# Optimization experiments

Hardware: AMD Instinct MI355X
Metric: run time of the kernel (lower is better)

## Reference

```python
import jax, jax.numpy as jnp
import numpy as np

B, N, D, H = 2, 2048, 1024, 16
HD = D // H
EPS = 1e-5

def _ln(x, g, b):
    m = jnp.mean(x, axis=-1, keepdims=True)
    v = jnp.mean((x - m) ** 2, axis=-1, keepdims=True)
    return (x - m) * jax.lax.rsqrt(v + EPS) * g + b

def setup_inputs() -> dict:
    key = jax.random.key(0)
    ks = jax.random.split(key, 16)
    s = 0.02
    inp = {
        'x': jax.random.normal(ks[0], (B, N, D), jnp.float32),
        'ln1_g': jnp.ones((D,), jnp.float32), 'ln1_b': jnp.zeros((D,), jnp.float32),
        'w_in': jax.random.normal(ks[1], (D, D), jnp.float32) * s, 'b_in': jnp.zeros((D,), jnp.float32),
        'wq': jax.random.normal(ks[2], (D, D), jnp.float32) * s,
        'wk': jax.random.normal(ks[3], (D, D), jnp.float32) * s,
        'wv': jax.random.normal(ks[4], (D, D), jnp.float32) * s,
        'wo': jax.random.normal(ks[5], (D, D), jnp.float32) * s, 'bo': jnp.zeros((D,), jnp.float32),
        'ln2_g': jnp.ones((D,), jnp.float32), 'ln2_b': jnp.zeros((D,), jnp.float32),
        'w_up': jax.random.normal(ks[6], (D, 4 * D), jnp.float32) * s, 'b_up': jnp.zeros((4 * D,), jnp.float32),
        'w_gate': jax.random.normal(ks[7], (D, 4 * D), jnp.float32) * s, 'b_gate': jnp.zeros((4 * D,), jnp.float32),
        'w_down': jax.random.normal(ks[8], (4 * D, D), jnp.float32) * s, 'b_down': jnp.zeros((D,), jnp.float32),
        'top_k': 64,
    }
    return inp

def _sparse_attention(h, wq, wk, wv, wo, bo, top_k):
    q = (h @ wq).reshape(B, N, H, HD).transpose(0, 2, 1, 3)  # [B,H,N,hd]
    k = (h @ wk).reshape(B, N, H, HD).transpose(0, 2, 1, 3)
    v = (h @ wv).reshape(B, N, H, HD).transpose(0, 2, 1, 3)
    scale = HD ** -0.5
    scores = jnp.einsum('bhqd,bhkd->bhqk', q, k) * scale  # [B,H,N,N]
    if top_k < N:
        # keep top_k per row: threshold at the k-th largest score
        kth = jax.lax.top_k(scores, top_k)[0][..., -1:]
        scores = jnp.where(scores >= kth, scores, -jnp.inf)
    attn = jax.nn.softmax(scores, axis=-1)
    out = jnp.einsum('bhqk,bhkd->bhqd', attn, v)
    out = out.transpose(0, 2, 1, 3).reshape(B, N, D)
    return out @ wo + bo

def reference(x, ln1_g, ln1_b, w_in, b_in, wq, wk, wv, wo, bo,
              ln2_g, ln2_b, w_up, b_up, w_gate, b_gate, w_down, b_down, top_k):
    h = _ln(x, ln1_g, ln1_b) @ w_in + b_in
    h = h + _sparse_attention(h, wq, wk, wv, wo, bo, top_k)
    ff_in = _ln(h, ln2_g, ln2_b)
    gate = jax.nn.silu(ff_in @ w_gate + b_gate)
    ff = (ff_in @ w_up + b_up) * gate
    ff = ff @ w_down + b_down
    return h + ff
```

## Files before the change

### kernel.cpp

```cpp
#include <hip/hip_runtime.h>
#include <cstdint>


#define DEV __device__ __forceinline__

constexpr int B_  = 2;
constexpr int N_  = 2048;
constexpr int D_  = 1024;
constexpr int H_  = 16;
constexpr int HD_ = 64;
constexpr int M_  = B_ * N_;
constexpr float EPS_ = 1e-5f;

using short8 = __attribute__((ext_vector_type(8))) short;
using f32x4  = __attribute__((ext_vector_type(4))) float;

DEV float4 ld4(const float* p) { return *reinterpret_cast<const float4*>(p); }
DEV void   st4(float* p, float4 v) { *reinterpret_cast<float4*>(p) = v; }

DEV unsigned short bf16r(float x) {
  unsigned u = __float_as_uint(x);
  u += 0x7fffu + ((u >> 16) & 1u);
  return (unsigned short)(u >> 16);
}
DEV float bf2f(unsigned short h) { return __uint_as_float(((unsigned)h) << 16); }

DEV unsigned fkey(float f) {
  unsigned u = __float_as_uint(f);
  return u ^ ((unsigned)((int)u >> 31) | 0x80000000u);
}
DEV float fval(unsigned k) {
  unsigned u = (k & 0x80000000u) ? (k ^ 0x80000000u) : ~k;
  return __uint_as_float(u);
}

__global__ __launch_bounds__(256) void wconv_kernel(const float* __restrict__ W,
                                                    unsigned short* __restrict__ Thi,
                                                    unsigned short* __restrict__ Tlo,
                                                    int K, int N) {
  __shared__ float t[32][33];
  const int k0 = blockIdx.y * 32, n0 = blockIdx.x * 32;
  const int tid = threadIdx.x;
  const int r = tid >> 3, c4 = (tid & 7) * 4;
  float4 v = ld4(W + (size_t)(k0 + r) * N + n0 + c4);
  t[r][c4 + 0] = v.x; t[r][c4 + 1] = v.y; t[r][c4 + 2] = v.z; t[r][c4 + 3] = v.w;
  __syncthreads();
  const int n = tid >> 3, kc = (tid & 7) * 4;
  ushort4 hv, lv;
  {
    float x0 = t[kc + 0][n], x1 = t[kc + 1][n], x2 = t[kc + 2][n], x3 = t[kc + 3][n];
    hv.x = bf16r(x0); lv.x = bf16r(x0 - bf2f(hv.x));
    hv.y = bf16r(x1); lv.y = bf16r(x1 - bf2f(hv.y));
    hv.z = bf16r(x2); lv.z = bf16r(x2 - bf2f(hv.z));
    hv.w = bf16r(x3); lv.w = bf16r(x3 - bf2f(hv.w));
  }
  *reinterpret_cast<ushort4*>(&Thi[(size_t)(n0 + n) * K + k0 + kc]) = hv;
  *reinterpret_cast<ushort4*>(&Tlo[(size_t)(n0 + n) * K + k0 + kc]) = lv;
}

__global__ __launch_bounds__(256) void ln_kernel(const float* __restrict__ in,
                                                 const float* __restrict__ g,
                                                 const float* __restrict__ b,
                                                 unsigned short* __restrict__ ohi,
                                                 unsigned short* __restrict__ olo) {
  const int row = blockIdx.x;
  const int t = threadIdx.x;
  float4 v = ld4(in + (size_t)row * D_ + t * 4);
  float s  = v.x + v.y + v.z + v.w;
  float ss = v.x * v.x + v.y * v.y + v.z * v.z + v.w * v.w;
  #pragma unroll
  for (int o = 32; o; o >>= 1) { s += __shfl_down(s, o); ss += __shfl_down(ss, o); }
  __shared__ float rs[4], rss[4];
  const int wid = t >> 6, lane = t & 63;
  if (lane == 0) { rs[wid] = s; rss[wid] = ss; }
  __syncthreads();
  s  = rs[0] + rs[1] + rs[2] + rs[3];
  ss = rss[0] + rss[1] + rss[2] + rss[3];
  const float mean = s * (1.f / D_);
  const float var  = ss * (1.f / D_) - mean * mean;
  const float rstd = rsqrtf(var + EPS_);
  float4 gv = ld4(g + t * 4);
  float4 bv = ld4(b + t * 4);
  float o0 = (v.x - mean) * rstd * gv.x + bv.x;
  float o1 = (v.y - mean) * rstd * gv.y + bv.y;
  float o2 = (v.z - mean) * rstd * gv.z + bv.z;
  float o3 = (v.w - mean) * rstd * gv.w + bv.w;
  ushort4 hv, lv;
  hv.x = bf16r(o0); lv.x = bf16r(o0 - bf2f(hv.x));
  hv.y = bf16r(o1); lv.y = bf16r(o1 - bf2f(hv.y));
  hv.z = bf16r(o2); lv.z = bf16r(o2 - bf2f(hv.z));
  hv.w = bf16r(o3); lv.w = bf16r(o3 - bf2f(hv.w));
  *reinterpret_cast<ushort4*>(&ohi[(size_t)row * D_ + t * 4]) = hv;
  *reinterpret_cast<ushort4*>(&olo[(size_t)row * D_ + t * 4]) = lv;
}

enum { GO_PAIR_BIAS = 0, GO_F32 = 1, GO_F32_BIAS_RESPAIR = 2,
       GO_F32_BIAS_RESF32 = 3, GO_F32_RES_NB = 4 };

template <int EPI>
__global__ __launch_bounds__(256) void gemm_sb(const unsigned short* __restrict__ Ah,
                                               const unsigned short* __restrict__ Al,
                                               const unsigned short* __restrict__ Bh,
                                               const unsigned short* __restrict__ Bl,
                                               const float* __restrict__ bias,
                                               const unsigned short* __restrict__ Rh,
                                               const unsigned short* __restrict__ Rl,
                                               const float* __restrict__ Rf,
                                               unsigned short* __restrict__ Ohi,
                                               unsigned short* __restrict__ Olo,
                                               float* __restrict__ Of,
                                               int M, int N, int K) {
  __shared__ unsigned short Ahs[128 * 40], Als[128 * 40];
  __shared__ unsigned short Bhs[64 * 40],  Bls[64 * 40];
  const int tid = threadIdx.x;
  const int m0 = blockIdx.y * 128, n0 = blockIdx.x * 64;
  const int lane = tid & 63, w = tid >> 6;
  const int wr = w >> 1, wc = w & 1;

  const int rA0 = tid >> 2, rA1 = 64 + (tid >> 2), chA = (tid & 3) * 8;
  const int rB = tid >> 2,  chB = (tid & 3) * 8;
  const size_t gA0 = (size_t)(m0 + rA0) * K + chA;
  const size_t gA1 = (size_t)(m0 + rA1) * K + chA;
  const size_t gB  = (size_t)(n0 + rB) * K + chB;
  const int lA0 = rA0 * 40 + chA, lA1 = rA1 * 40 + chA, lB = rB * 40 + chB;

  f32x4 acc[4][2];
  #pragma unroll
  for (int i = 0; i < 4; ++i)
    #pragma unroll
    for (int j = 0; j < 2; ++j) acc[i][j] = f32x4{0.f, 0.f, 0.f, 0.f};

  const int fr = lane & 15, fk = (lane >> 4) * 8;
  const int arow0 = (wr * 64 + fr) * 40 + fk;
  const int brow0 = (wc * 32 + fr) * 40 + fk;

  for (int k0 = 0; k0 < K; k0 += 32) {
    short8 a0h = *reinterpret_cast<const short8*>(&Ah[gA0 + k0]);
    short8 a1h = *reinterpret_cast<const short8*>(&Ah[gA1 + k0]);
    short8 a0l = *reinterpret_cast<const short8*>(&Al[gA0 + k0]);
    short8 a1l = *reinterpret_cast<const short8*>(&Al[gA1 + k0]);
    short8 bh  = *reinterpret_cast<const short8*>(&Bh[gB + k0]);
    short8 bl  = *reinterpret_cast<const short8*>(&Bl[gB + k0]);
    __syncthreads();
    *reinterpret_cast<short8*>(&Ahs[lA0]) = a0h;
    *reinterpret_cast<short8*>(&Ahs[lA1]) = a1h;
    *reinterpret_cast<short8*>(&Als[lA0]) = a0l;
    *reinterpret_cast<short8*>(&Als[lA1]) = a1l;
    *reinterpret_cast<short8*>(&Bhs[lB])  = bh;
    *reinterpret_cast<short8*>(&Bls[lB])  = bl;
    __syncthreads();

    short8 amh[4], aml[4], bnh[2], bnl[2];
    #pragma unroll
    for (int mf = 0; mf < 4; ++mf) {
      amh[mf] = *reinterpret_cast<const short8*>(&Ahs[arow0 + mf * 16 * 40]);
      aml[mf] = *reinterpret_cast<const short8*>(&Als[arow0 + mf * 16 * 40]);
    }
    #pragma unroll
    for (int nf = 0; nf < 2; ++nf) {
      bnh[nf] = *reinterpret_cast<const short8*>(&Bhs[brow0 + nf * 16 * 40]);
      bnl[nf] = *reinterpret_cast<const short8*>(&Bls[brow0 + nf * 16 * 40]);
    }
    #pragma unroll
    for (int mf = 0; mf < 4; ++mf)
      #pragma unroll
      for (int nf = 0; nf < 2; ++nf) {
        acc[mf][nf] = __builtin_amdgcn_mfma_f32_16x16x32_bf16(amh[mf], bnh[nf], acc[mf][nf], 0, 0, 0);
        acc[mf][nf] = __builtin_amdgcn_mfma_f32_16x16x32_bf16(amh[mf], bnl[nf], acc[mf][nf], 0, 0, 0);
        acc[mf][nf] = __builtin_amdgcn_mfma_f32_16x16x32_bf16(aml[mf], bnh[nf], acc[mf][nf], 0, 0, 0);
      }
  }

  const int er = (lane >> 4) * 4, ec = lane & 15;
  #pragma unroll
  for (int mf = 0; mf < 4; ++mf)
    #pragma unroll
    for (int nf = 0; nf < 2; ++nf)
      #pragma unroll
      for (int j = 0; j < 4; ++j) {
        const int m = m0 + wr * 64 + mf * 16 + er + j;
        const int n = n0 + wc * 32 + nf * 16 + ec;
        float v = acc[mf][nf][j];
        if constexpr (EPI == GO_PAIR_BIAS || EPI == GO_F32_BIAS_RESPAIR ||
                      EPI == GO_F32_BIAS_RESF32) v += bias[n];
        const size_t idx = (size_t)m * N + n;
        if constexpr (EPI == GO_PAIR_BIAS) {
          unsigned short h = bf16r(v);
          Ohi[idx] = h; Olo[idx] = bf16r(v - bf2f(h));
        } else if constexpr (EPI == GO_F32) {
          Of[idx] = v;
        } else if constexpr (EPI == GO_F32_BIAS_RESPAIR) {
          Of[idx] = v + bf2f(Rh[idx]) + bf2f(Rl[idx]);
        } else {
          Of[idx] = v + Rf[idx];
        }
      }
}

__global__ __launch_bounds__(256) void gemm_gateup(const unsigned short* __restrict__ Ah,
                                                   const unsigned short* __restrict__ Al,
                                                   const unsigned short* __restrict__ Gh,
                                                   const unsigned short* __restrict__ Gl,
                                                   const unsigned short* __restrict__ Uh,
                                                   const unsigned short* __restrict__ Ul,
                                                   const float* __restrict__ bg,
                                                   const float* __restrict__ bu,
                                                   unsigned short* __restrict__ Ohi,
                                                   unsigned short* __restrict__ Olo,
                                                   int M, int N, int K) {
  __shared__ unsigned short Ahs[128 * 40], Als[128 * 40];
  __shared__ unsigned short Ghs[64 * 40], Gls[64 * 40], Uhs[64 * 40], Uls[64 * 40];
  const int tid = threadIdx.x;
  const int m0 = blockIdx.y * 128, n0 = blockIdx.x * 64;
  const int lane = tid & 63, w = tid >> 6;
  const int wr = w >> 1, wc = w & 1;

  const int rA0 = tid >> 2, rA1 = 64 + (tid >> 2), chA = (tid & 3) * 8;
  const int rB = tid >> 2, chB = (tid & 3) * 8;
  const size_t gA0 = (size_t)(m0 + rA0) * K + chA;
  const size_t gA1 = (size_t)(m0 + rA1) * K + chA;
  const size_t gB  = (size_t)(n0 + rB) * K + chB;
  const int lA0 = rA0 * 40 + chA, lA1 = rA1 * 40 + chA, lB = rB * 40 + chB;

  f32x4 accg[4][2], accu[4][2];
  #pragma unroll
  for (int i = 0; i < 4; ++i)
    #pragma unroll
    for (int j = 0; j < 2; ++j) {
      accg[i][j] = f32x4{0.f, 0.f, 0.f, 0.f};
      accu[i][j] = f32x4{0.f, 0.f, 0.f, 0.f};
    }

  const int fr = lane & 15, fk = (lane >> 4) * 8;
  const int arow0 = (wr * 64 + fr) * 40 + fk;
  const int brow0 = (wc * 32 + fr) * 40 + fk;

  for (int k0 = 0; k0 < K; k0 += 32) {
    short8 a0h = *reinterpret_cast<const short8*>(&Ah[gA0 + k0]);
    short8 a1h = *reinterpret_cast<const short8*>(&Ah[gA1 + k0]);
    short8 a0l = *reinterpret_cast<const short8*>(&Al[gA0 + k0]);
    short8 a1l = *reinterpret_cast<const short8*>(&Al[gA1 + k0]);
    short8 gh = *reinterpret_cast<const short8*>(&Gh[gB + k0]);
    short8 gl = *reinterpret_cast<const short8*>(&Gl[gB + k0]);
    short8 uh = *reinterpret_cast<const short8*>(&Uh[gB + k0]);
    short8 ul = *reinterpret_cast<const short8*>(&Ul[gB + k0]);
    __syncthreads();
    *reinterpret_cast<short8*>(&Ahs[lA0]) = a0h;
    *reinterpret_cast<short8*>(&Ahs[lA1]) = a1h;
    *reinterpret_cast<short8*>(&Als[lA0]) = a0l;
    *reinterpret_cast<short8*>(&Als[lA1]) = a1l;
    *reinterpret_cast<short8*>(&Ghs[lB]) = gh;
    *reinterpret_cast<short8*>(&Gls[lB]) = gl;
    *reinterpret_cast<short8*>(&Uhs[lB]) = uh;
    *reinterpret_cast<short8*>(&Uls[lB]) = ul;
    __syncthreads();

    short8 amh[4], aml[4];
    #pragma unroll
    for (int mf = 0; mf < 4; ++mf) {
      amh[mf] = *reinterpret_cast<const short8*>(&Ahs[arow0 + mf * 16 * 40]);
      aml[mf] = *reinterpret_cast<const short8*>(&Als[arow0 + mf * 16 * 40]);
    }
    #pragma unroll
    for (int nf = 0; nf < 2; ++nf) {
      short8 gnh = *reinterpret_cast<const short8*>(&Ghs[brow0 + nf * 16 * 40]);
      short8 gnl = *reinterpret_cast<const short8*>(&Gls[brow0 + nf * 16 * 40]);
      short8 unh = *reinterpret_cast<const short8*>(&Uhs[brow0 + nf * 16 * 40]);
      short8 unl = *reinterpret_cast<const short8*>(&Uls[brow0 + nf * 16 * 40]);
      #pragma unroll
      for (int mf = 0; mf < 4; ++mf) {
        accg[mf][nf] = __builtin_amdgcn_mfma_f32_16x16x32_bf16(amh[mf], gnh, accg[mf][nf], 0, 0, 0);
        accg[mf][nf] = __builtin_amdgcn_mfma_f32_16x16x32_bf16(amh[mf], gnl, accg[mf][nf], 0, 0, 0);
        accg[mf][nf] = __builtin_amdgcn_mfma_f32_16x16x32_bf16(aml[mf], gnh, accg[mf][nf], 0, 0, 0);
        accu[mf][nf] = __builtin_amdgcn_mfma_f32_16x16x32_bf16(amh[mf], unh, accu[mf][nf], 0, 0, 0);
        accu[mf][nf] = __builtin_amdgcn_mfma_f32_16x16x32_bf16(amh[mf], unl, accu[mf][nf], 0, 0, 0);
        accu[mf][nf] = __builtin_amdgcn_mfma_f32_16x16x32_bf16(aml[mf], unh, accu[mf][nf], 0, 0, 0);
      }
    }
  }

  const int er = (lane >> 4) * 4, ec = lane & 15;
  #pragma unroll
  for (int mf = 0; mf < 4; ++mf)
    #pragma unroll
    for (int nf = 0; nf < 2; ++nf)
      #pragma unroll
      for (int j = 0; j < 4; ++j) {
        const int m = m0 + wr * 64 + mf * 16 + er + j;
        const int n = n0 + wc * 32 + nf * 16 + ec;
        float g = accg[mf][nf][j] + bg[n];
        float u = accu[mf][nf][j] + bu[n];
        float f = (g / (1.f + expf(-g))) * u;
        const size_t idx = (size_t)m * N + n;
        unsigned short h = bf16r(f);
        Ohi[idx] = h; Olo[idx] = bf16r(f - bf2f(h));
      }
}

__global__ __launch_bounds__(256) void attn_kernel(const float* __restrict__ qm,
                                                   const float* __restrict__ km,
                                                   const float* __restrict__ vm,
                                                   unsigned short* __restrict__ aoh,
                                                   unsigned short* __restrict__ aol,
                                                   const int* __restrict__ topk_p) {
  constexpr int QT = 4, CT = 128, NCH = N_ / CT;
  constexpr int NJ = 2 * NCH;
  __shared__ float Kc[CT][HD_];
  __shared__ float Pt[4][QT][CT];
  int*   selIdx = (int*)&Pt[0][0][0];
  float* selW   = (float*)&Pt[2][0][0];

  const int tid = threadIdx.x;
  const int bid = ((blockIdx.x & 7) << 11) | (blockIdx.x >> 3);
  const int qt = bid & (N_ / QT - 1);
  const int hh = (bid >> 9) & (H_ - 1);
  const int bb = bid >> 13;
  const int q0 = qt * QT;
  const size_t baseKV = (size_t)bb * N_ * D_ + (size_t)hh * HD_;
  const int lane = tid & 63;
  const int w = tid >> 6;
  const float scale = 0.125f;

  float4 qr[QT][4];
  #pragma unroll
  for (int r = 0; r < QT; ++r)
    #pragma unroll
    for (int dq = 0; dq < 4; ++dq) {
      float4 t = ld4(qm + baseKV + (size_t)(q0 + r) * D_ + w * 16 + dq * 4);
      t.x *= scale; t.y *= scale; t.z *= scale; t.w *= scale;
      qr[r][dq] = t;
    }

  unsigned key[NJ];
  for (int cb = 0; cb < NCH; ++cb) {
    float4 kst[8];
    #pragma unroll
    for (int it = 0; it < 8; ++it) {
      const int c = it * 16 + (tid >> 4);
      kst[it] = ld4(km + baseKV + (size_t)(cb * CT + c) * D_ + (tid & 15) * 4);
    }
    __syncthreads();
    #pragma unroll
    for (int it = 0; it < 8; ++it) {
      const int c = it * 16 + (tid >> 4);
      const int chk = (tid & 15) ^ (c & 15);
      st4(&Kc[c][chk * 4], kst[it]);
    }
    __syncthreads();

    float pa[QT][2];
    #pragma unroll
    for (int r = 0; r < QT; ++r) { pa[r][0] = 0.f; pa[r][1] = 0.f; }
    #pragma unroll
    for (int dq = 0; dq < 4; ++dq) {
      const int ch = w * 4 + dq;
      float4 k0 = ld4(&Kc[lane][(ch ^ (lane & 15)) * 4]);
      float4 k1 = ld4(&Kc[lane + 64][(ch ^ (lane & 15)) * 4]);
      #pragma unroll
      for (int r = 0; r < QT; ++r) {
        float4 qv = qr[r][dq];
        pa[r][0] += qv.x * k0.x + qv.y * k0.y + qv.z * k0.z + qv.w * k0.w;
        pa[r][1] += qv.x * k1.x + qv.y * k1.y + qv.z * k1.z + qv.w * k1.w;
      }
    }
    #pragma unroll
    for (int r = 0; r < QT; ++r) {
      Pt[w][r][lane]      = pa[r][0];
      Pt[w][r][lane + 64] = pa[r][1];
    }
    __syncthreads();
    {
      float s0 = Pt[0][w][lane] + Pt[1][w][lane] + Pt[2][w][lane] + Pt[3][w][lane];
      float s1 = Pt[0][w][lane + 64] + Pt[1][w][lane + 64] +
                 Pt[2][w][lane + 64] + Pt[3][w][lane + 64];
      key[2 * cb]     = fkey(s0);
      key[2 * cb + 1] = fkey(s1);
    }
  }

  int topk = *topk_p;
  if (topk > N_) topk = N_;

  unsigned kmax = 0;
  #pragma unroll
  for (int j = 0; j < NJ; ++j) kmax = (key[j] > kmax) ? key[j] : kmax;
  #pragma unroll
  for (int o = 32; o; o >>= 1) {
    unsigned t = __shfl_xor(kmax, o);
    kmax = (t > kmax) ? t : kmax;
  }
  const float smax = fval(kmax);

  unsigned thr = 0u;
  if (topk < N_) {
    for (int bit = 31; bit >= 0; --bit) {
      const unsigned cand = thr | (1u << bit);
      int c = 0;
      #pragma unroll
      for (int j = 0; j < NJ; ++j)
        c += __popcll(__ballot(key[j] >= cand));
      if (c >= topk) thr = cand;
    }
  }

  __syncthreads();
  int base = 0;
  float wpart = 0.f;
  #pragma unroll
  for (int j = 0; j < NJ; ++j) {
    const bool sel = key[j] >= thr;
    const unsigned long long m = __ballot(sel);
    if (sel) {
      const int pos = base + (int)__popcll(m & ((1ull << lane) - 1ull));
      if (pos < 128) {
        const float wgt = expf(fval(key[j]) - smax);
        selIdx[w * 128 + pos] = j * 64 + lane;
        selW[w * 128 + pos] = wgt;
        wpart += wgt;
      }
    }
    base += (int)__popcll(m);
  }
  int cnt = (base > 128) ? 128 : base;
  float wsum = wpart;
  #pragma unroll
  for (int o = 32; o; o >>= 1) wsum += __shfl_xor(wsum, o);

  const float* Vb = vm + baseKV;
  float outv = 0.f;
  int i = 0;
  for (; i + 16 <= cnt; i += 16) {
    int ix[16]; float wv[16], vv[16];
    #pragma unroll
    for (int t = 0; t < 16; ++t) {
      ix[t] = selIdx[w * 128 + i + t];
      wv[t] = selW[w * 128 + i + t];
    }
    #pragma unroll
    for (int t = 0; t < 16; ++t) vv[t] = Vb[(size_t)ix[t] * D_ + lane];
    #pragma unroll
    for (int t = 0; t < 16; ++t) outv += wv[t] * vv[t];
  }
  for (; i < cnt; ++i)
    outv += selW[w * 128 + i] * Vb[(size_t)selIdx[w * 128 + i] * D_ + lane];

  const float o = outv / wsum;
  const size_t oidx = ((size_t)bb * N_ + q0 + w) * D_ + hh * HD_ + lane;
  unsigned short h = bf16r(o);
  aoh[oidx] = h; aol[oidx] = bf16r(o - bf2f(h));
}

extern "C" void kernel_launch(void* const* d_in, const int* in_sizes, int n_in,
                              void* d_out, int out_size, void* d_ws, size_t ws_size,
                              hipStream_t stream) {
  const float* x      = (const float*)d_in[0];
  const float* ln1_g  = (const float*)d_in[1];
  const float* ln1_b  = (const float*)d_in[2];
  const float* w_in   = (const float*)d_in[3];
  const float* b_in   = (const float*)d_in[4];
  const float* wq     = (const float*)d_in[5];
  const float* wk     = (const float*)d_in[6];
  const float* wv     = (const float*)d_in[7];
  const float* wo     = (const float*)d_in[8];
  const float* bo     = (const float*)d_in[9];
  const float* ln2_g  = (const float*)d_in[10];
  const float* ln2_b  = (const float*)d_in[11];
  const float* w_up   = (const float*)d_in[12];
  const float* b_up   = (const float*)d_in[13];
  const float* w_gate = (const float*)d_in[14];
  const float* b_gate = (const float*)d_in[15];
  const float* w_down = (const float*)d_in[16];
  const float* b_down = (const float*)d_in[17];
  const int*   topk   = (const int*)d_in[18];
  float* out = (float*)d_out;

  char* p = (char*)d_ws;
  const size_t MB = 1024 * 1024;
  unsigned short* Wi_h = (unsigned short*)(p + 0 * MB);
  unsigned short* Wi_l = (unsigned short*)(p + 2 * MB);
  unsigned short* Wq_h = (unsigned short*)(p + 4 * MB);
  unsigned short* Wq_l = (unsigned short*)(p + 6 * MB);
  unsigned short* Wk_h = (unsigned short*)(p + 8 * MB);
  unsigned short* Wk_l = (unsigned short*)(p + 10 * MB);
  unsigned short* Wv_h = (unsigned short*)(p + 12 * MB);
  unsigned short* Wv_l = (unsigned short*)(p + 14 * MB);
  unsigned short* Wo_h = (unsigned short*)(p + 16 * MB);
  unsigned short* Wo_l = (unsigned short*)(p + 18 * MB);
  unsigned short* Wd0_h = (unsigned short*)(p + 20 * MB);
  unsigned short* Wd0_l = (unsigned short*)(p + 24 * MB);
  unsigned short* Wd1_h = (unsigned short*)(p + 28 * MB);
  unsigned short* Wd1_l = (unsigned short*)(p + 32 * MB);
  unsigned short* hp_h = (unsigned short*)(p + 36 * MB);
  unsigned short* hp_l = (unsigned short*)(p + 44 * MB);
  unsigned short* ff_h = (unsigned short*)(p + 36 * MB);
  unsigned short* ff_l = (unsigned short*)(p + 44 * MB);
  unsigned short* xn_h = (unsigned short*)(p + 52 * MB);
  unsigned short* xn_l = (unsigned short*)(p + 60 * MB);
  float*          qb   = (float*)(p + 52 * MB);
  float*          kb   = (float*)(p + 68 * MB);
  float*          vb   = (float*)(p + 84 * MB);
  unsigned short* Wg_h = (unsigned short*)(p + 52 * MB);
  unsigned short* Wg_l = (unsigned short*)(p + 60 * MB);
  unsigned short* Wu_h = (unsigned short*)(p + 68 * MB);
  unsigned short* Wu_l = (unsigned short*)(p + 76 * MB);
  unsigned short* f1_h = (unsigned short*)(p + 84 * MB);
  unsigned short* ao_h = (unsigned short*)(p + 0 * MB);
  unsigned short* ao_l = (unsigned short*)(p + 8 * MB);
  unsigned short* f1_l = (unsigned short*)(p + 0 * MB);

  const dim3 blk(256);
  const dim3 gW1k(32, 32);
  const dim3 gWgu(128, 32);
  const dim3 gWd(32, 64);
  const dim3 g1024(16, 32);
  const dim3 g2048(32, 32);

  wconv_kernel<<<gW1k, blk, 0, stream>>>(w_in, Wi_h, Wi_l, 1024, 1024);
  wconv_kernel<<<gW1k, blk, 0, stream>>>(wq, Wq_h, Wq_l, 1024, 1024);
  wconv_kernel<<<gW1k, blk, 0, stream>>>(wk, Wk_h, Wk_l, 1024, 1024);
  wconv_kernel<<<gW1k, blk, 0, stream>>>(wv, Wv_h, Wv_l, 1024, 1024);
  wconv_kernel<<<gW1k, blk, 0, stream>>>(wo, Wo_h, Wo_l, 1024, 1024);
  wconv_kernel<<<gWd, blk, 0, stream>>>(w_down,               Wd0_h, Wd0_l, 2048, 1024);
  wconv_kernel<<<gWd, blk, 0, stream>>>(w_down + 2048 * 1024, Wd1_h, Wd1_l, 2048, 1024);

  ln_kernel<<<M_, blk, 0, stream>>>(x, ln1_g, ln1_b, xn_h, xn_l);
  gemm_sb<GO_PAIR_BIAS><<<g1024, blk, 0, stream>>>(xn_h, xn_l, Wi_h, Wi_l, b_in,
      nullptr, nullptr, nullptr, hp_h, hp_l, nullptr, M_, 1024, 1024);
  gemm_sb<GO_F32><<<g1024, blk, 0, stream>>>(hp_h, hp_l, Wq_h, Wq_l, nullptr,
      nullptr, nullptr, nullptr, nullptr, nullptr, qb, M_, 1024, 1024);
  gemm_sb<GO_F32><<<g1024, blk, 0, stream>>>(hp_h, hp_l, Wk_h, Wk_l, nullptr,
      nullptr, nullptr, nullptr, nullptr, nullptr, kb, M_, 1024, 1024);
  gemm_sb<GO_F32><<<g1024, blk, 0, stream>>>(hp_h, hp_l, Wv_h, Wv_l, nullptr,
      nullptr, nullptr, nullptr, nullptr, nullptr, vb, M_, 1024, 1024);

  attn_kernel<<<B_ * H_ * (N_ / 4), blk, 0, stream>>>(qb, kb, vb, ao_h, ao_l, topk);

  wconv_kernel<<<gWgu, blk, 0, stream>>>(w_gate, Wg_h, Wg_l, 1024, 4096);
  wconv_kernel<<<gWgu, blk, 0, stream>>>(w_up,   Wu_h, Wu_l, 1024, 4096);

  gemm_sb<GO_F32_BIAS_RESPAIR><<<g1024, blk, 0, stream>>>(ao_h, ao_l, Wo_h, Wo_l, bo,
      hp_h, hp_l, nullptr, nullptr, nullptr, out, M_, 1024, 1024);

  ln_kernel<<<M_, blk, 0, stream>>>(out, ln2_g, ln2_b, ff_h, ff_l);

  gemm_gateup<<<g2048, blk, 0, stream>>>(ff_h, ff_l,
      Wg_h, Wg_l, Wu_h, Wu_l, b_gate, b_up, f1_h, f1_l, M_, 2048, 1024);
  gemm_sb<GO_F32_BIAS_RESF32><<<g1024, blk, 0, stream>>>(f1_h, f1_l, Wd0_h, Wd0_l,
      b_down, nullptr, nullptr, out, nullptr, nullptr, out, M_, 1024, 2048);
  gemm_gateup<<<g2048, blk, 0, stream>>>(ff_h, ff_l,
      Wg_h + (size_t)2048 * 1024, Wg_l + (size_t)2048 * 1024,
      Wu_h + (size_t)2048 * 1024, Wu_l + (size_t)2048 * 1024,
      b_gate + 2048, b_up + 2048, f1_h, f1_l, M_, 2048, 1024);
  gemm_sb<GO_F32_RES_NB><<<g1024, blk, 0, stream>>>(f1_h, f1_l, Wd1_h, Wd1_l,
      nullptr, nullptr, nullptr, out, nullptr, nullptr, out, M_, 1024, 2048);
}
```

Before: 1.516 ms.

## Compute attention scores with split-bf16 MFMA over 16-query tiles

Q and K projections now emit hi/lo bf16 pairs, and the attention kernel computes QK^T with 3-term split-bf16 MFMA instead of fp32 FMA through an LDS K tile. Each block handles 16 queries per head instead of 4, so K is read from global memory a quarter as often. Scores are staged through LDS in four passes to build per-row selection keys. The radix threshold search can also stop early once the count equals top_k exactly. In exchange, the kernel holds 32 f32x4 accumulators and 128 keys per thread, which means high register pressure and lower occupancy. The split-bf16 product is also slightly less exact than fp32.

```diff
diff --git a/kernel.cpp b/kernel.cpp
--- a/kernel.cpp
+++ b/kernel.cpp
@@ -95,7 +95,7 @@
 }
 
 enum { GO_PAIR_BIAS = 0, GO_F32 = 1, GO_F32_BIAS_RESPAIR = 2,
-       GO_F32_BIAS_RESF32 = 3, GO_F32_RES_NB = 4 };
+       GO_F32_BIAS_RESF32 = 3, GO_F32_RES_NB = 4, GO_PAIR_NB = 5 };
 
 template <int EPI>
 __global__ __launch_bounds__(256) void gemm_sb(const unsigned short* __restrict__ Ah,
@@ -184,7 +184,7 @@
         if constexpr (EPI == GO_PAIR_BIAS || EPI == GO_F32_BIAS_RESPAIR ||
                       EPI == GO_F32_BIAS_RESF32) v += bias[n];
         const size_t idx = (size_t)m * N + n;
-        if constexpr (EPI == GO_PAIR_BIAS) {
+        if constexpr (EPI == GO_PAIR_BIAS || EPI == GO_PAIR_NB) {
           unsigned short h = bf16r(v);
           Ohi[idx] = h; Olo[idx] = bf16r(v - bf2f(h));
         } else if constexpr (EPI == GO_F32) {
@@ -297,157 +297,162 @@
       }
 }
 
-__global__ __launch_bounds__(256) void attn_kernel(const float* __restrict__ qm,
-                                                   const float* __restrict__ km,
-                                                   const float* __restrict__ vm,
-                                                   unsigned short* __restrict__ aoh,
-                                                   unsigned short* __restrict__ aol,
-                                                   const int* __restrict__ topk_p) {
-  constexpr int QT = 4, CT = 128, NCH = N_ / CT;
-  constexpr int NJ = 2 * NCH;
-  __shared__ float Kc[CT][HD_];
-  __shared__ float Pt[4][QT][CT];
-  int*   selIdx = (int*)&Pt[0][0][0];
-  float* selW   = (float*)&Pt[2][0][0];
+__global__ __launch_bounds__(256) void attn_kernel(
+    const unsigned short* __restrict__ qh, const unsigned short* __restrict__ ql,
+    const unsigned short* __restrict__ kh, const unsigned short* __restrict__ kl,
+    const float* __restrict__ vm,
+    unsigned short* __restrict__ aoh, unsigned short* __restrict__ aol,
+    const int* __restrict__ topk_p) {
+  constexpr int QB = 16;
+  constexpr int NJ = N_ / 64;
+  __shared__ float Sb[QB][513];
+  __shared__ int   selIdx[4][128];
+  __shared__ float selS[4][128];
 
   const int tid = threadIdx.x;
-  const int bid = ((blockIdx.x & 7) << 11) | (blockIdx.x >> 3);
-  const int qt = bid & (N_ / QT - 1);
-  const int hh = (bid >> 9) & (H_ - 1);
-  const int bb = bid >> 13;
-  const int q0 = qt * QT;
-  const size_t baseKV = (size_t)bb * N_ * D_ + (size_t)hh * HD_;
-  const int lane = tid & 63;
-  const int w = tid >> 6;
-  const float scale = 0.125f;
-
-  float4 qr[QT][4];
-  #pragma unroll
-  for (int r = 0; r < QT; ++r)
-    #pragma unroll
-    for (int dq = 0; dq < 4; ++dq) {
-      float4 t = ld4(qm + baseKV + (size_t)(q0 + r) * D_ + w * 16 + dq * 4);
-      t.x *= scale; t.y *= scale; t.z *= scale; t.w *= scale;
-      qr[r][dq] = t;
-    }
-
-  unsigned key[NJ];
-  for (int cb = 0; cb < NCH; ++cb) {
-    float4 kst[8];
-    #pragma unroll
-    for (int it = 0; it < 8; ++it) {
-      const int c = it * 16 + (tid >> 4);
-      kst[it] = ld4(km + baseKV + (size_t)(cb * CT + c) * D_ + (tid & 15) * 4);
+  const int lane = tid & 63, w = tid >> 6;
+  const int bid = ((blockIdx.x & 7) << 9) | (blockIdx.x >> 3);
+  const int qt = bid & 127;
+  const int hh = (bid >> 7) & (H_ - 1);
+  const int bb = bid >> 11;
+  const int q0 = qt * QB;
+
+  const int fr = lane & 15;
+  const int fk = (lane >> 4) * 8;
+
+  const size_t qbase = ((size_t)(bb * N_ + q0 + fr)) * D_ + hh * HD_ + fk;
+  short8 ah0 = *reinterpret_cast<const short8*>(qh + qbase);
+  short8 ah1 = *reinterpret_cast<const short8*>(qh + qbase + 32);
+  short8 al0 = *reinterpret_cast<const short8*>(ql + qbase);
+  short8 al1 = *reinterpret_cast<const short8*>(ql + qbase + 32);
+
+  const int c0 = w * 512;
+  const size_t kwb = ((size_t)(bb * N_ + c0 + fr)) * D_ + hh * HD_ + fk;
+
+  f32x4 acc[32];
+  #pragma unroll
+  for (int ct = 0; ct < 32; ++ct) acc[ct] = f32x4{0.f, 0.f, 0.f, 0.f};
+
+  #pragma unroll
+  for (int ct = 0; ct < 32; ++ct) {
+    const size_t kb0 = kwb + (size_t)ct * 16 * D_;
+    short8 bh0 = *reinterpret_cast<const short8*>(kh + kb0);
+    short8 bh1 = *reinterpret_cast<const short8*>(kh + kb0 + 32);
+    short8 bl0 = *reinterpret_cast<const short8*>(kl + kb0);
+    short8 bl1 = *reinterpret_cast<const short8*>(kl + kb0 + 32);
+    acc[ct] = __builtin_amdgcn_mfma_f32_16x16x32_bf16(ah0, bh0, acc[ct], 0, 0, 0);
+    acc[ct] = __builtin_amdgcn_mfma_f32_16x16x32_bf16(ah0, bl0, acc[ct], 0, 0, 0);
+    acc[ct] = __builtin_amdgcn_mfma_f32_16x16x32_bf16(al0, bh0, acc[ct], 0, 0, 0);
+    acc[ct] = __builtin_amdgcn_mfma_f32_16x16x32_bf16(ah1, bh1, acc[ct], 0, 0, 0);
+    acc[ct] = __builtin_amdgcn_mfma_f32_16x16x32_bf16(ah1, bl1, acc[ct], 0, 0, 0);
+    acc[ct] = __builtin_amdgcn_mfma_f32_16x16x32_bf16(al1, bh1, acc[ct], 0, 0, 0);
+  }
+
+  unsigned key[4][NJ];
+  const int r0 = (lane >> 4) * 4;
+  #pragma unroll
+  for (int c = 0; c < 4; ++c) {
+    if (w == c) {
+      #pragma unroll
+      for (int ct = 0; ct < 32; ++ct) {
+        const int col = ct * 16 + fr;
+        #pragma unroll
+        for (int j = 0; j < 4; ++j)
+          Sb[r0 + j][col] = acc[ct][j] * 0.125f;
+      }
     }
     __syncthreads();
     #pragma unroll
-    for (int it = 0; it < 8; ++it) {
-      const int c = it * 16 + (tid >> 4);
-      const int chk = (tid & 15) ^ (c & 15);
-      st4(&Kc[c][chk * 4], kst[it]);
+    for (int rr = 0; rr < 4; ++rr) {
+      const int row = w + rr * 4;
+      #pragma unroll
+      for (int jj = 0; jj < 8; ++jj)
+        key[rr][c * 8 + jj] = fkey(Sb[row][jj * 64 + lane]);
     }
     __syncthreads();
-
-    float pa[QT][2];
-    #pragma unroll
-    for (int r = 0; r < QT; ++r) { pa[r][0] = 0.f; pa[r][1] = 0.f; }
-    #pragma unroll
-    for (int dq = 0; dq < 4; ++dq) {
-      const int ch = w * 4 + dq;
-      float4 k0 = ld4(&Kc[lane][(ch ^ (lane & 15)) * 4]);
-      float4 k1 = ld4(&Kc[lane + 64][(ch ^ (lane & 15)) * 4]);
-      #pragma unroll
-      for (int r = 0; r < QT; ++r) {
-        float4 qv = qr[r][dq];
-        pa[r][0] += qv.x * k0.x + qv.y * k0.y + qv.z * k0.z + qv.w * k0.w;
-        pa[r][1] += qv.x * k1.x + qv.y * k1.y + qv.z * k1.z + qv.w * k1.w;
-      }
-    }
-    #pragma unroll
-    for (int r = 0; r < QT; ++r) {
-      Pt[w][r][lane]      = pa[r][0];
-      Pt[w][r][lane + 64] = pa[r][1];
-    }
-    __syncthreads();
-    {
-      float s0 = Pt[0][w][lane] + Pt[1][w][lane] + Pt[2][w][lane] + Pt[3][w][lane];
-      float s1 = Pt[0][w][lane + 64] + Pt[1][w][lane + 64] +
-                 Pt[2][w][lane + 64] + Pt[3][w][lane + 64];
-      key[2 * cb]     = fkey(s0);
-      key[2 * cb + 1] = fkey(s1);
-    }
   }
 
   int topk = *topk_p;
   if (topk > N_) topk = N_;
-
-  unsigned kmax = 0;
-  #pragma unroll
-  for (int j = 0; j < NJ; ++j) kmax = (key[j] > kmax) ? key[j] : kmax;
-  #pragma unroll
-  for (int o = 32; o; o >>= 1) {
-    unsigned t = __shfl_xor(kmax, o);
-    kmax = (t > kmax) ? t : kmax;
+  const float* Vb = vm + (size_t)bb * N_ * D_ + hh * HD_;
+
+  #pragma unroll
+  for (int rr = 0; rr < 4; ++rr) {
+    unsigned kmax = 0;
+    #pragma unroll
+    for (int j = 0; j < NJ; ++j) kmax = (key[rr][j] > kmax) ? key[rr][j] : kmax;
+    #pragma unroll
+    for (int o = 32; o; o >>= 1) {
+      unsigned t = __shfl_xor(kmax, o);
+      kmax = (t > kmax) ? t : kmax;
+    }
+    const float smax = fval(kmax);
+
+    unsigned thr = 0u;
+    if (topk < N_) {
+      for (int bit = 31; bit >= 0; --bit) {
+        const unsigned cand = thr | (1u << bit);
+        int c = 0;
+        #pragma unroll
+        for (int j = 0; j < NJ; ++j)
+          c += __popcll(__ballot(key[rr][j] >= cand));
+        if (c >= topk) {
+          thr = cand;
+          if (c == topk) break;
+        }
+      }
+    }
+
+    int base = 0;
+    #pragma unroll
+    for (int j = 0; j < NJ; ++j) {
+      const bool sel = key[rr][j] >= thr;
+      const unsigned long long m = __ballot(sel);
+      if (sel) {
+        const int pos = base + (int)__popcll(m & ((1ull << lane) - 1ull));
+        if (pos < 128) {
+          selIdx[w][pos] = j * 64 + lane;
+          selS[w][pos]   = fval(key[rr][j]);
+        }
+      }
+      base += (int)__popcll(m);
+    }
+    const int cnt = (base > 128) ? 128 : base;
+
+    float wsum = 0.f;
+    if (lane < cnt) {
+      float e = expf(selS[w][lane] - smax);
+      selS[w][lane] = e; wsum += e;
+    }
+    if (lane + 64 < cnt) {
+      float e = expf(selS[w][lane + 64] - smax);
+      selS[w][lane + 64] = e; wsum += e;
+    }
+    #pragma unroll
+    for (int o = 32; o; o >>= 1) wsum += __shfl_xor(wsum, o);
+
+    float outv = 0.f;
+    int i = 0;
+    for (; i + 16 <= cnt; i += 16) {
+      int ix[16]; float wv[16], vv[16];
+      #pragma unroll
+      for (int t = 0; t < 16; ++t) {
+        ix[t] = selIdx[w][i + t];
+        wv[t] = selS[w][i + t];
+      }
+      #pragma unroll
+      for (int t = 0; t < 16; ++t) vv[t] = Vb[(size_t)ix[t] * D_ + lane];
+      #pragma unroll
+      for (int t = 0; t < 16; ++t) outv += wv[t] * vv[t];
+    }
+    for (; i < cnt; ++i)
+      outv += selS[w][i] * Vb[(size_t)selIdx[w][i] * D_ + lane];
+
+    const float o = outv / wsum;
+    const size_t oidx = ((size_t)bb * N_ + q0 + w + rr * 4) * D_ + hh * HD_ + lane;
+    unsigned short hsh = bf16r(o);
+    aoh[oidx] = hsh; aol[oidx] = bf16r(o - bf2f(hsh));
   }
-  const float smax = fval(kmax);
-
-  unsigned thr = 0u;
-  if (topk < N_) {
-    for (int bit = 31; bit >= 0; --bit) {
-      const unsigned cand = thr | (1u << bit);
-      int c = 0;
-      #pragma unroll
-      for (int j = 0; j < NJ; ++j)
-        c += __popcll(__ballot(key[j] >= cand));
-      if (c >= topk) thr = cand;
-    }
-  }
-
-  __syncthreads();
-  int base = 0;
-  float wpart = 0.f;
-  #pragma unroll
-  for (int j = 0; j < NJ; ++j) {
-    const bool sel = key[j] >= thr;
-    const unsigned long long m = __ballot(sel);
-    if (sel) {
-      const int pos = base + (int)__popcll(m & ((1ull << lane) - 1ull));
-      if (pos < 128) {
-        const float wgt = expf(fval(key[j]) - smax);
-        selIdx[w * 128 + pos] = j * 64 + lane;
-        selW[w * 128 + pos] = wgt;
-        wpart += wgt;
-      }
-    }
-    base += (int)__popcll(m);
-  }
-  int cnt = (base > 128) ? 128 : base;
-  float wsum = wpart;
-  #pragma unroll
-  for (int o = 32; o; o >>= 1) wsum += __shfl_xor(wsum, o);
-
-  const float* Vb = vm + baseKV;
-  float outv = 0.f;
-  int i = 0;
-  for (; i + 16 <= cnt; i += 16) {
-    int ix[16]; float wv[16], vv[16];
-    #pragma unroll
-    for (int t = 0; t < 16; ++t) {
-      ix[t] = selIdx[w * 128 + i + t];
-      wv[t] = selW[w * 128 + i + t];
-    }
-    #pragma unroll
-    for (int t = 0; t < 16; ++t) vv[t] = Vb[(size_t)ix[t] * D_ + lane];
-    #pragma unroll
-    for (int t = 0; t < 16; ++t) outv += wv[t] * vv[t];
-  }
-  for (; i < cnt; ++i)
-    outv += selW[w * 128 + i] * Vb[(size_t)selIdx[w * 128 + i] * D_ + lane];
-
-  const float o = outv / wsum;
-  const size_t oidx = ((size_t)bb * N_ + q0 + w) * D_ + hh * HD_ + lane;
-  unsigned short h = bf16r(o);
-  aoh[oidx] = h; aol[oidx] = bf16r(o - bf2f(h));
 }
 
 extern "C" void kernel_launch(void* const* d_in, const int* in_sizes, int n_in,
@@ -496,8 +501,10 @@
   unsigned short* ff_l = (unsigned short*)(p + 44 * MB);
   unsigned short* xn_h = (unsigned short*)(p + 52 * MB);
   unsigned short* xn_l = (unsigned short*)(p + 60 * MB);
-  float*          qb   = (float*)(p + 52 * MB);
-  float*          kb   = (float*)(p + 68 * MB);
+  unsigned short* q_h  = (unsigned short*)(p + 52 * MB);
+  unsigned short* q_l  = (unsigned short*)(p + 60 * MB);
+  unsigned short* k_h  = (unsigned short*)(p + 68 * MB);
+  unsigned short* k_l  = (unsigned short*)(p + 76 * MB);
   float*          vb   = (float*)(p + 84 * MB);
   unsigned short* Wg_h = (unsigned short*)(p + 52 * MB);
   unsigned short* Wg_l = (unsigned short*)(p + 60 * MB);
@@ -526,14 +533,15 @@
   ln_kernel<<<M_, blk, 0, stream>>>(x, ln1_g, ln1_b, xn_h, xn_l);
   gemm_sb<GO_PAIR_BIAS><<<g1024, blk, 0, stream>>>(xn_h, xn_l, Wi_h, Wi_l, b_in,
       nullptr, nullptr, nullptr, hp_h, hp_l, nullptr, M_, 1024, 1024);
-  gemm_sb<GO_F32><<<g1024, blk, 0, stream>>>(hp_h, hp_l, Wq_h, Wq_l, nullptr,
-      nullptr, nullptr, nullptr, nullptr, nullptr, qb, M_, 1024, 1024);
-  gemm_sb<GO_F32><<<g1024, blk, 0, stream>>>(hp_h, hp_l, Wk_h, Wk_l, nullptr,
-      nullptr, nullptr, nullptr, nullptr, nullptr, kb, M_, 1024, 1024);
+  gemm_sb<GO_PAIR_NB><<<g1024, blk, 0, stream>>>(hp_h, hp_l, Wq_h, Wq_l, nullptr,
+      nullptr, nullptr, nullptr, q_h, q_l, nullptr, M_, 1024, 1024);
+  gemm_sb<GO_PAIR_NB><<<g1024, blk, 0, stream>>>(hp_h, hp_l, Wk_h, Wk_l, nullptr,
+      nullptr, nullptr, nullptr, k_h, k_l, nullptr, M_, 1024, 1024);
   gemm_sb<GO_F32><<<g1024, blk, 0, stream>>>(hp_h, hp_l, Wv_h, Wv_l, nullptr,
       nullptr, nullptr, nullptr, nullptr, nullptr, vb, M_, 1024, 1024);
 
-  attn_kernel<<<B_ * H_ * (N_ / 4), blk, 0, stream>>>(qb, kb, vb, ao_h, ao_l, topk);
+  attn_kernel<<<B_ * H_ * (N_ / 16), blk, 0, stream>>>(q_h, q_l, k_h, k_l, vb,
+      ao_h, ao_l, topk);
 
   wconv_kernel<<<gWgu, blk, 0, stream>>>(w_gate, Wg_h, Wg_l, 1024, 4096);
   wconv_kernel<<<gWgu, blk, 0, stream>>>(w_up,   Wu_h, Wu_l, 1024, 4096);
```

After: 1.333 ms. -12.1%, faster.
